# Kernel optimization log

Measured on AMD Instinct MI355X. Metric: run time of the kernel, lower is better.

## Reference

```python
import jax, jax.numpy as jnp
import numpy as np

BATCH = 8192
IN_FEATURES = 4096
OUT_FEATURES = 4096
TT_RANK = 8
IN_MODES = (16, 16, 16)
OUT_MODES = (16, 16, 16)


def setup_inputs() -> dict:
    key = jax.random.key(0)
    ks = jax.random.split(key, 5)
    # core std ~ glorot-ish scale for TT factors
    std = 0.05
    x = jax.random.normal(ks[0], (BATCH, IN_FEATURES), dtype=jnp.float32)
    core0 = std * jax.random.normal(ks[1], (1, OUT_MODES[0], IN_MODES[0], TT_RANK), dtype=jnp.float32)
    core1 = std * jax.random.normal(ks[2], (TT_RANK, OUT_MODES[1], IN_MODES[1], TT_RANK), dtype=jnp.float32)
    core2 = std * jax.random.normal(ks[3], (TT_RANK, OUT_MODES[2], IN_MODES[2], 1), dtype=jnp.float32)
    bias = 0.001 * jnp.ones((OUT_FEATURES,), dtype=jnp.float32)
    return {"x": x, "core0": core0, "core1": core1, "core2": core2, "bias": bias}


def _tt_dense_matmul(cores, b):
    """A @ b where A (out_features x in_features) is in TT-matrix format.
    cores[k]: (r_k, o_k, i_k, r_{k+1}), r_0 = r_d = 1. b: (in_features, batch).
    Returns (out_features, batch). Mirrors t3nsor/t3f tt_dense_matmul."""
    in_dims = [c.shape[2] for c in cores]
    ranks = [c.shape[0] for c in cores] + [cores[-1].shape[3]]
    out_features = int(np.prod([c.shape[1] for c in cores]))
    data = b.T                                   # (batch, in_features)
    data = data.reshape(-1, in_dims[-1], 1)      # (batch*prod(i[:-1]), i_last, r_d=1)
    for k in range(len(cores) - 1, -1, -1):
        # core (a=r_k, i=o_k, j=i_k, b=r_{k+1}); data (r, j, b) -> (i, r, a)
        data = jnp.einsum('aijb,rjb->ira', cores[k], data)
        if k > 0:
            data = data.reshape(-1, in_dims[k - 1], ranks[k])
    return data.reshape(out_features, -1)        # (out_features, batch)


def reference(x, core0, core1, core2, bias):
    # forward: tt_dense_matmul(weight_t, x^T)^T + bias
    y = _tt_dense_matmul([core0, core1, core2], x.T)  # (out_features, batch)
    return y.T + bias                                 # (batch, out_features)
```

## Files before the change

kernel.cpp:

```cpp
#include <hip/hip_runtime.h>
#include <cstdint>


typedef __bf16 bf16x8 __attribute__((ext_vector_type(8)));
typedef float f32x4 __attribute__((ext_vector_type(4)));
typedef unsigned short u16;
typedef u16 u16x8 __attribute__((ext_vector_type(8)));

__device__ __forceinline__ u16 f2bf(float f) {
    unsigned u = __builtin_bit_cast(unsigned, f);
    u += 0x7fffu + ((u >> 16) & 1u);
    return (u16)(u >> 16);
}

__global__ void k_cvt(const float* __restrict__ x, u16* __restrict__ xb) {
    long i = (long)blockIdx.x * blockDim.x + threadIdx.x;
    const float4* p = (const float4*)x;
    float4 a = p[2 * i], b = p[2 * i + 1];
    u16x8 o;
    o[0] = f2bf(a.x); o[1] = f2bf(a.y); o[2] = f2bf(a.z); o[3] = f2bf(a.w);
    o[4] = f2bf(b.x); o[5] = f2bf(b.y); o[6] = f2bf(b.z); o[7] = f2bf(b.w);
    ((u16x8*)xb)[i] = o;
}

__global__ void k_c01(const float* __restrict__ c0, const float* __restrict__ c1,
                      float* __restrict__ c01) {
    int idx = blockIdx.x * 256 + threadIdx.x;
    int b2 = idx & 7, i1 = (idx >> 3) & 15, i0 = (idx >> 7) & 15;
    int o1 = (idx >> 11) & 15, o0 = idx >> 15;
    float s = 0.f;
#pragma unroll
    for (int b1 = 0; b1 < 8; ++b1)
        s += c0[(o0 * 16 + i0) * 8 + b1] * c1[((b1 * 16 + o1) * 16 + i1) * 8 + b2];
    c01[idx] = s;
}

__global__ void k_w(const float* __restrict__ c01, const float* __restrict__ c2,
                    u16* __restrict__ wbt) {
    int idx = blockIdx.x * 256 + threadIdx.x;
    int i2h = idx & 1;
    int i1 = (idx >> 1) & 15;
    int i0 = (idx >> 5) & 15;
    int o = idx >> 9;
    int o2 = o & 15, o1 = (o >> 4) & 15, o0 = o >> 8;
    const float* c = &c01[(((o0 * 16 + o1) * 16 + i0) * 16 + i1) * 8];
    float acc[8] = {0, 0, 0, 0, 0, 0, 0, 0};
#pragma unroll
    for (int b2 = 0; b2 < 8; ++b2) {
        float cv = c[b2];
        const float* cc = &c2[(b2 * 16 + o2) * 16 + i2h * 8];
#pragma unroll
        for (int j = 0; j < 8; ++j) acc[j] += cv * cc[j];
    }
    u16x8 ov;
#pragma unroll
    for (int j = 0; j < 8; ++j) ov[j] = f2bf(acc[j]);
    ((u16x8*)wbt)[(long)o * 512 + (i0 * 32 + i1 * 2 + i2h)] = ov;
}

#define BM 256
#define BN 256
#define BK 64
#define TILEU (BM * BK)
#define LDS_BYTES (4 * TILEU * 2)

static_assert(LDS_BYTES == 131072, "lds size");

__device__ __forceinline__ void gload_lds16(const void* g, void* l) {
    __builtin_amdgcn_global_load_lds(
        (const __attribute__((address_space(1))) unsigned*)g,
        (__attribute__((address_space(3))) unsigned*)l, 16, 0, 0);
}

#define VMW(N) asm volatile("s_waitcnt vmcnt(" #N ")" ::: "memory")
#define LGKM0  asm volatile("s_waitcnt lgkmcnt(0)" ::: "memory")
#define BAR()  __builtin_amdgcn_s_barrier()

#define READ_A(H) do { \
    _Pragma("unroll") for (int mi_ = 0; mi_ < 4; ++mi_) { \
        af[mi_ * 2 + 0] = *(const bf16x8*)&aT[arow + ((H) * 128 + mi_ * 16) * 64 + swz0]; \
        af[mi_ * 2 + 1] = *(const bf16x8*)&aT[arow + ((H) * 128 + mi_ * 16) * 64 + swz1]; \
    } } while (0)

#define READ_B(G, BF) do { \
    _Pragma("unroll") for (int ni_ = 0; ni_ < 2; ++ni_) { \
        BF[ni_ * 2 + 0] = *(const bf16x8*)&bT[brow + ((G) * 128 + ni_ * 16) * 64 + swz0]; \
        BF[ni_ * 2 + 1] = *(const bf16x8*)&bT[brow + ((G) * 128 + ni_ * 16) * 64 + swz1]; \
    } } while (0)

#define MFMA16(H, G, BF) do { \
    __builtin_amdgcn_s_setprio(1); \
    _Pragma("unroll") for (int mi_ = 0; mi_ < 4; ++mi_) \
    _Pragma("unroll") for (int ni_ = 0; ni_ < 2; ++ni_) \
    _Pragma("unroll") for (int kk_ = 0; kk_ < 2; ++kk_) \
        acc[(H) * 4 + mi_][(G) * 2 + ni_] = __builtin_amdgcn_mfma_f32_16x16x32_bf16( \
            af[mi_ * 2 + kk_], BF[ni_ * 2 + kk_], acc[(H) * 4 + mi_][(G) * 2 + ni_], 0, 0, 0); \
    __builtin_amdgcn_s_setprio(0); \
} while (0)

#define TILE(BUF, TT, PRE, W1, W2, W4) do { \
    const u16* aT = lds + (BUF) * TILEU; \
    const u16* bT = lds + 2 * TILEU + (BUF) * TILEU; \
    u16* sA = lds + (1 - (BUF)) * TILEU; \
    u16* sB = lds + 2 * TILEU + (1 - (BUF)) * TILEU; \
    const long ko = (long)((TT) + 1) * BK; \
     \
    if (PRE) { gload_lds16(pa[0] + ko, sA + t * 8); \
               gload_lds16(pa[1] + ko, sA + 4096 + t * 8); } \
    READ_A(0); READ_B(0, bf0); \
    BAR(); LGKM0; \
    MFMA16(0, 0, bf0); \
    W1; BAR(); \
     \
    if (PRE) { gload_lds16(pb[0] + ko, sB + t * 8); \
               gload_lds16(pb[1] + ko, sB + 4096 + t * 8); } \
    READ_B(1, bf1); \
    BAR(); LGKM0; \
    MFMA16(0, 1, bf1); \
    W2; BAR(); \
     \
    if (PRE) { gload_lds16(pb[2] + ko, sB + 8192 + t * 8); \
               gload_lds16(pb[3] + ko, sB + 12288 + t * 8); } \
    READ_A(1); \
    BAR(); LGKM0; \
    MFMA16(1, 1, bf1); \
    BAR(); \
     \
    if (PRE) { gload_lds16(pa[2] + ko, sA + 8192 + t * 8); \
               gload_lds16(pa[3] + ko, sA + 12288 + t * 8); } \
    MFMA16(1, 0, bf0); \
    W4; BAR(); \
} while (0)

__launch_bounds__(512, 2)
__global__ void k_gemm(const u16* __restrict__ A, const u16* __restrict__ B,
                       const float* __restrict__ bias, float* __restrict__ C,
                       int M, int N, int K) {
    extern __shared__ __align__(16) u16 lds[];

    const int wg = blockIdx.x;
    const int swzb = (wg & 7) * 64 + (wg >> 3);
    const int bn = swzb & 15, bm = swzb >> 4;
    const int m0 = bm * BM, n0 = bn * BN;

    const int t = threadIdx.x;
    const int wave = t >> 6, lane = t & 63;
    const int wm = wave >> 2, wn = wave & 3;
    const int lr = lane & 15, quad = lane >> 4;

    const u16 *pa[4], *pb[4];
#pragma unroll
    for (int j = 0; j < 4; ++j) {
        int ci = j * 512 + t;
        int lrow = ci >> 3;
        int c = (ci & 7) ^ (lrow & 7);
        int rA = ((lrow >> 6) & 1) * 128 + (lrow >> 7) * 64 + (lrow & 63);
        int rB = ((lrow >> 5) & 3) * 64 + (lrow >> 7) * 32 + (lrow & 31);
        pa[j] = &A[(long)(m0 + rA) * K + c * 8];
        pb[j] = &B[(long)(n0 + rB) * K + c * 8];
    }

    const int swz0 = ((quad    ) ^ (lr & 7)) * 8;
    const int swz1 = ((quad + 4) ^ (lr & 7)) * 8;
    const int arow = (wm * 64 + lr) * 64;
    const int brow = (wn * 32 + lr) * 64;

    f32x4 acc[8][4];
#pragma unroll
    for (int mi = 0; mi < 8; ++mi)
#pragma unroll
        for (int ni = 0; ni < 4; ++ni) acc[mi][ni] = 0.f;

    bf16x8 af[8], bf0[4], bf1[4];

    gload_lds16(pa[0], lds + t * 8);
    gload_lds16(pa[1], lds + 4096 + t * 8);
    gload_lds16(pb[0], lds + 2 * TILEU + t * 8);
    gload_lds16(pb[1], lds + 2 * TILEU + 4096 + t * 8);
    gload_lds16(pb[2], lds + 2 * TILEU + 8192 + t * 8);
    gload_lds16(pb[3], lds + 2 * TILEU + 12288 + t * 8);
    gload_lds16(pa[2], lds + 8192 + t * 8);
    gload_lds16(pa[3], lds + 12288 + t * 8);
    VMW(4); BAR();

#pragma unroll 1
    for (int tt = 0; tt < 62; tt += 2) {
        TILE(0, tt,     1, VMW(4), VMW(4), VMW(4));
        TILE(1, tt + 1, 1, VMW(4), VMW(4), VMW(4));
    }
    TILE(0, 62, 1, VMW(4), VMW(4), VMW(4));
    TILE(1, 63, 0, VMW(2), VMW(0), );

#pragma unroll
    for (int ni = 0; ni < 4; ++ni) {
        int gn = n0 + wn * 64 + ni * 16 + lr;
        float bv = bias[gn];
#pragma unroll
        for (int mi = 0; mi < 8; ++mi) {
            int gm = m0 + wm * 128 + mi * 16 + quad * 4;
#pragma unroll
            for (int r = 0; r < 4; ++r)
                C[(long)(gm + r) * N + gn] = acc[mi][ni][r] + bv;
        }
    }
}

extern "C" void kernel_launch(void* const* d_in, const int* in_sizes, int n_in,
                              void* d_out, int out_size, void* d_ws, size_t ws_size,
                              hipStream_t stream) {
    const float* x = (const float*)d_in[0];
    const float* c0 = (const float*)d_in[1];
    const float* c1 = (const float*)d_in[2];
    const float* c2 = (const float*)d_in[3];
    const float* bias = (const float*)d_in[4];
    float* out = (float*)d_out;

    const int Mb = 8192, Nf = 4096, Kf = 4096;
    char* ws = (char*)d_ws;
    u16* xb = (u16*)ws;
    u16* wbt = (u16*)(ws + 67108864);
    float* c01 = (float*)(ws + 67108864 + 33554432);

    hipFuncSetAttribute(reinterpret_cast<const void*>(k_gemm),
                        hipFuncAttributeMaxDynamicSharedMemorySize, LDS_BYTES);

    k_cvt<<<dim3((Mb * Kf / 8) / 256), 256, 0, stream>>>(x, xb);
    k_c01<<<dim3(2048), 256, 0, stream>>>(c0, c1, c01);
    k_w<<<dim3(8192), 256, 0, stream>>>(c01, c2, wbt);
    k_gemm<<<dim3((Mb / BM) * (Nf / BN)), dim3(512), LDS_BYTES, stream>>>(
        xb, wbt, bias, out, Mb, Nf, Kf);
}
```

Baseline: 464.5 us.

## Software-pipeline LDS fragment reads across tiles and cut barriers in GEMM loop

The GEMM main loop is restructured so the A and B register fragments for the next K tile are read from LDS while the current tile's MFMAs are still issuing. Global-to-LDS prefetches are grouped into two batches of four, and the number of s_barriers per tile drops from four to two, with sched_barrier fences keeping the MFMA blocks in order. The goal is to hide LDS read latency and reduce synchronisation stalls between waves. The cost is more complex waitcnt/barrier reasoning, with some risk of LDS races if a prefetch overwrites a buffer another wave is still reading, plus a full vmcnt(0) drain in the prologue.

```diff
diff --git a/kernel.cpp b/kernel.cpp
--- a/kernel.cpp
+++ b/kernel.cpp
@@ -75,30 +75,31 @@
 #define VMW(N) asm volatile("s_waitcnt vmcnt(" #N ")" ::: "memory")
 #define LGKM0  asm volatile("s_waitcnt lgkmcnt(0)" ::: "memory")
 #define BAR()  __builtin_amdgcn_s_barrier()
-
-#define READ_A(H) do { \
+#define SCHED0 __builtin_amdgcn_sched_barrier(0)
+
+#define READ_A(H, DST, BASE) do { \
     _Pragma("unroll") for (int mi_ = 0; mi_ < 4; ++mi_) { \
-        af[mi_ * 2 + 0] = *(const bf16x8*)&aT[arow + ((H) * 128 + mi_ * 16) * 64 + swz0]; \
-        af[mi_ * 2 + 1] = *(const bf16x8*)&aT[arow + ((H) * 128 + mi_ * 16) * 64 + swz1]; \
+        DST[mi_ * 2 + 0] = *(const bf16x8*)&(BASE)[arow + ((H) * 128 + mi_ * 16) * 64 + swz0]; \
+        DST[mi_ * 2 + 1] = *(const bf16x8*)&(BASE)[arow + ((H) * 128 + mi_ * 16) * 64 + swz1]; \
     } } while (0)
 
-#define READ_B(G, BF) do { \
+#define READ_B(G, DST, BASE) do { \
     _Pragma("unroll") for (int ni_ = 0; ni_ < 2; ++ni_) { \
-        BF[ni_ * 2 + 0] = *(const bf16x8*)&bT[brow + ((G) * 128 + ni_ * 16) * 64 + swz0]; \
-        BF[ni_ * 2 + 1] = *(const bf16x8*)&bT[brow + ((G) * 128 + ni_ * 16) * 64 + swz1]; \
+        DST[ni_ * 2 + 0] = *(const bf16x8*)&(BASE)[brow + ((G) * 128 + ni_ * 16) * 64 + swz0]; \
+        DST[ni_ * 2 + 1] = *(const bf16x8*)&(BASE)[brow + ((G) * 128 + ni_ * 16) * 64 + swz1]; \
     } } while (0)
 
-#define MFMA16(H, G, BF) do { \
+#define MFMA16(ASET, BF, H, G) do { \
     __builtin_amdgcn_s_setprio(1); \
     _Pragma("unroll") for (int mi_ = 0; mi_ < 4; ++mi_) \
     _Pragma("unroll") for (int ni_ = 0; ni_ < 2; ++ni_) \
     _Pragma("unroll") for (int kk_ = 0; kk_ < 2; ++kk_) \
         acc[(H) * 4 + mi_][(G) * 2 + ni_] = __builtin_amdgcn_mfma_f32_16x16x32_bf16( \
-            af[mi_ * 2 + kk_], BF[ni_ * 2 + kk_], acc[(H) * 4 + mi_][(G) * 2 + ni_], 0, 0, 0); \
+            ASET[mi_ * 2 + kk_], BF[ni_ * 2 + kk_], acc[(H) * 4 + mi_][(G) * 2 + ni_], 0, 0, 0); \
     __builtin_amdgcn_s_setprio(0); \
 } while (0)
 
-#define TILE(BUF, TT, PRE, W1, W2, W4) do { \
+#define TILE(BUF, TT, PRE) do { \
     const u16* aT = lds + (BUF) * TILEU; \
     const u16* bT = lds + 2 * TILEU + (BUF) * TILEU; \
     u16* sA = lds + (1 - (BUF)) * TILEU; \
@@ -106,30 +107,30 @@
     const long ko = (long)((TT) + 1) * BK; \
      \
     if (PRE) { gload_lds16(pa[0] + ko, sA + t * 8); \
-               gload_lds16(pa[1] + ko, sA + 4096 + t * 8); } \
-    READ_A(0); READ_B(0, bf0); \
-    BAR(); LGKM0; \
-    MFMA16(0, 0, bf0); \
-    W1; BAR(); \
-     \
-    if (PRE) { gload_lds16(pb[0] + ko, sB + t * 8); \
+               gload_lds16(pa[1] + ko, sA + 4096 + t * 8); \
+               gload_lds16(pb[0] + ko, sB + t * 8); \
                gload_lds16(pb[1] + ko, sB + 4096 + t * 8); } \
-    READ_B(1, bf1); \
-    BAR(); LGKM0; \
-    MFMA16(0, 1, bf1); \
-    W2; BAR(); \
+    LGKM0; SCHED0; \
+    MFMA16(aA, b0, 0, 0); \
+    if (PRE) { VMW(4); } else { VMW(0); } \
+    BAR(); \
+    READ_B(1, b1, bT); \
      \
     if (PRE) { gload_lds16(pb[2] + ko, sB + 8192 + t * 8); \
-               gload_lds16(pb[3] + ko, sB + 12288 + t * 8); } \
-    READ_A(1); \
-    BAR(); LGKM0; \
-    MFMA16(1, 1, bf1); \
-    BAR(); \
-     \
-    if (PRE) { gload_lds16(pa[2] + ko, sA + 8192 + t * 8); \
+               gload_lds16(pb[3] + ko, sB + 12288 + t * 8); \
+               gload_lds16(pa[2] + ko, sA + 8192 + t * 8); \
                gload_lds16(pa[3] + ko, sA + 12288 + t * 8); } \
-    MFMA16(1, 0, bf0); \
-    W4; BAR(); \
+    LGKM0; SCHED0; \
+    MFMA16(aA, b1, 0, 1); \
+    READ_A(1, aA, aT); \
+     \
+    if (PRE) { VMW(4); BAR(); } \
+    LGKM0; SCHED0; \
+    MFMA16(aA, b0, 1, 0); \
+    if (PRE) { READ_B(0, b0, sB); } \
+     \
+    MFMA16(aA, b1, 1, 1); \
+    if (PRE) { READ_A(0, aA, sA); } \
 } while (0)
 
 __launch_bounds__(512, 2)
@@ -171,7 +172,7 @@
 #pragma unroll
         for (int ni = 0; ni < 4; ++ni) acc[mi][ni] = 0.f;
 
-    bf16x8 af[8], bf0[4], bf1[4];
+    bf16x8 aA[8], b0[4], b1[4];
 
     gload_lds16(pa[0], lds + t * 8);
     gload_lds16(pa[1], lds + 4096 + t * 8);
@@ -181,15 +182,17 @@
     gload_lds16(pb[3], lds + 2 * TILEU + 12288 + t * 8);
     gload_lds16(pa[2], lds + 8192 + t * 8);
     gload_lds16(pa[3], lds + 12288 + t * 8);
-    VMW(4); BAR();
+    VMW(0); BAR();
+    READ_A(0, aA, lds);
+    READ_B(0, b0, (lds + 2 * TILEU));
 
 #pragma unroll 1
     for (int tt = 0; tt < 62; tt += 2) {
-        TILE(0, tt,     1, VMW(4), VMW(4), VMW(4));
-        TILE(1, tt + 1, 1, VMW(4), VMW(4), VMW(4));
-    }
-    TILE(0, 62, 1, VMW(4), VMW(4), VMW(4));
-    TILE(1, 63, 0, VMW(2), VMW(0), );
+        TILE(0, tt,     1);
+        TILE(1, tt + 1, 1);
+    }
+    TILE(0, 62, 1);
+    TILE(1, 63, 0);
 
 #pragma unroll
     for (int ni = 0; ni < 4; ++ni) {
```

Result: no change. 471.3 us (+1.5%).
